# Kernel tuning notes

Hardware: AMD Instinct MI355X
Metric: run time of the kernel (lower is better)

## Reference

```python
import jax, jax.numpy as jnp
import numpy as np

N_NODES = 50000
N_EDGES = 800000
D = 64  # node_in = edge_out = node_out

def _mlp(h, w1, b1, w2, b2):
    h = jax.nn.relu(h @ w1 + b1)
    return h @ w2 + b2

def setup_inputs() -> dict:
    key = jax.random.key(0)
    ks = jax.random.split(key, 12)
    def lin(k, fan_in, fan_out):
        bound = 1.0 / np.sqrt(fan_in)
        kw, kb = jax.random.split(k)
        w = jax.random.uniform(kw, (fan_in, fan_out), jnp.float32, -bound, bound)
        b = jax.random.uniform(kb, (fan_out,), jnp.float32, -bound, bound)
        return w, b
    x = jax.random.normal(ks[0], (N_NODES, D), jnp.float32)
    edge_index = jax.random.randint(ks[1], (2, N_EDGES), 0, N_NODES, jnp.int64 if jax.config.jax_enable_x64 else jnp.int32)
    edge_attr = jax.random.normal(ks[2], (N_EDGES, D), jnp.float32)
    u = jax.random.normal(ks[3], (1, D), jnp.float32)
    batch = jnp.zeros((N_NODES,), dtype=edge_index.dtype)
    w1a, b1a = lin(ks[4], 2 * D, D)
    w1b, b1b = lin(ks[5], D, D)
    w2a, b2a = lin(ks[6], 2 * D, D)
    w2b, b2b = lin(ks[7], D, D)
    return dict(x=x, edge_index=edge_index, edge_attr=edge_attr, u=u, batch=batch,
                w1a=w1a, b1a=b1a, w1b=w1b, b1b=b1b,
                w2a=w2a, b2a=b2a, w2b=w2b, b2b=b2b)

def reference(x, edge_index, edge_attr, u, batch,
              w1a, b1a, w1b, b1b, w2a, b2a, w2b, b2b):
    row, col = edge_index[0], edge_index[1]
    n = x.shape[0]
    # gather source nodes, concat with edge features: [E, node_in+edge_out]
    h = jnp.concatenate([x[row], edge_attr], axis=1)
    h = _mlp(h, w1a, b1a, w1b, b1b)
    # scatter_mean over destination nodes (zeros for nodes with no incoming edges)
    summed = jax.ops.segment_sum(h, col, num_segments=n)  # [N, D]
    counts = jax.ops.segment_sum(jnp.ones((h.shape[0],), h.dtype), col, num_segments=n)
    agg = summed / jnp.maximum(counts, 1.0)[:, None]
    out = jnp.concatenate([x, agg], axis=1)
    return _mlp(out, w2a, b2a, w2b, b2b)
```

## Files before the change

kernel.cpp:

```cpp
#include <hip/hip_runtime.h>

#define DF 64

typedef __attribute__((ext_vector_type(8))) short bf16x8;
typedef __attribute__((ext_vector_type(2))) short v2s;
typedef __attribute__((ext_vector_type(4))) float f32x4;

__device__ __forceinline__ short f2bf(float f) {
    union { float f; unsigned u; } v; v.f = f;
    unsigned u = v.u;
    u += 0x7FFFu + ((u >> 16) & 1u);
    return (short)(u >> 16);
}

__device__ __forceinline__ float bf2f(unsigned s) {
    union { unsigned u; float f; } v; v.u = s << 16;
    return v.f;
}

__device__ __forceinline__ bf16x8 cvt8(float4 a, float4 b) {
    bf16x8 r;
    r[0] = f2bf(a.x); r[1] = f2bf(a.y); r[2] = f2bf(a.z); r[3] = f2bf(a.w);
    r[4] = f2bf(b.x); r[5] = f2bf(b.y); r[6] = f2bf(b.z); r[7] = f2bf(b.w);
    return r;
}

__device__ __forceinline__ void pk_add(short* addr, int val) {
#if __has_builtin(__builtin_amdgcn_global_atomic_fadd_v2bf16)
    __builtin_amdgcn_global_atomic_fadd_v2bf16(
        (__attribute__((address_space(1))) v2s*)addr, *(v2s*)&val);
#else
    unsigned* a = (unsigned*)addr;
    unsigned old = *a, assumed;
    do {
        assumed = old;
        float lo = bf2f(assumed & 0xffffu) + bf2f((unsigned)val & 0xffffu);
        float hi = bf2f(assumed >> 16)     + bf2f((unsigned)val >> 16);
        unsigned nv = (unsigned)(unsigned short)f2bf(lo) |
                      ((unsigned)(unsigned short)f2bf(hi) << 16);
        old = atomicCAS(a, assumed, nv);
    } while (old != assumed);
#endif
}

__global__ __launch_bounds__(256) void prep_weights(
    const float* __restrict__ w1a, const float* __restrict__ w1b,
    const float* __restrict__ w2a, const float* __restrict__ w2b,
    short* __restrict__ w1aT, short* __restrict__ w1bT,
    short* __restrict__ w2aT, short* __restrict__ w2bT)
{
    int gid = blockIdx.x * 256 + threadIdx.x;
    if (gid < 8192) {
        int k = gid >> 6, n = gid & 63;
        w1aT[n * 128 + k] = f2bf(w1a[gid]);
    } else if (gid < 12288) {
        int g = gid - 8192; int k = g >> 6, n = g & 63;
        w1bT[n * 64 + k] = f2bf(w1b[g]);
    } else if (gid < 20480) {
        int g = gid - 12288; int k = g >> 6, n = g & 63;
        w2aT[n * 128 + k] = f2bf(w2a[g]);
    } else if (gid < 24576) {
        int g = gid - 20480; int k = g >> 6, n = g & 63;
        w2bT[n * 64 + k] = f2bf(w2b[g]);
    }
}

__global__ __launch_bounds__(256, 8) void edge_mlp_scatter(
    const float* __restrict__ x, const int* __restrict__ ei,
    const float* __restrict__ ea,
    const short* __restrict__ w1aT, const float* __restrict__ b1a,
    const short* __restrict__ w1bT, const float* __restrict__ b1b,
    short* __restrict__ summedh, float* __restrict__ counts, int E)
{
    __shared__ alignas(16) short lsH[4 * 16 * 72];

    const int t = threadIdx.x;
    const int lane = t & 63;
    const int w = t >> 6;
    const int q = lane >> 4;
    const int m = lane & 15;
    const long base = ((long)blockIdx.x * 4 + w) * 16;

    const long e = base + m;
    const long ec = e < E ? e : (long)(E - 1);
    const int row = ei[ec];

    if (q == 0 && e < E)
        unsafeAtomicAdd(&counts[ei[E + e]], 1.0f);

    const float4* xr = (const float4*)(x + (long)row * DF);
    const float4* er = (const float4*)(ea + ec * DF);
    bf16x8 afr[4];
    afr[0] = cvt8(xr[q * 2],     xr[q * 2 + 1]);
    afr[1] = cvt8(xr[8 + q * 2], xr[8 + q * 2 + 1]);
    afr[2] = cvt8(er[q * 2],     er[q * 2 + 1]);
    afr[3] = cvt8(er[8 + q * 2], er[8 + q * 2 + 1]);

    f32x4 acc[4];
#pragma unroll
    for (int nt = 0; nt < 4; ++nt) {
        float b = b1a[nt * 16 + m];
        f32x4 v = {b, b, b, b};
        acc[nt] = v;
#pragma unroll
        for (int ks = 0; ks < 4; ++ks) {
            bf16x8 bfr = *(const bf16x8*)&w1aT[(nt * 16 + m) * 128 + ks * 32 + q * 8];
            acc[nt] = __builtin_amdgcn_mfma_f32_16x16x32_bf16(afr[ks], bfr, acc[nt], 0, 0, 0);
        }
    }

    short* hw = lsH + w * (16 * 72);
#pragma unroll
    for (int nt = 0; nt < 4; ++nt)
#pragma unroll
        for (int r = 0; r < 4; ++r) {
            float v = acc[nt][r] > 0.f ? acc[nt][r] : 0.f;
            hw[(q * 4 + r) * 72 + nt * 16 + m] = f2bf(v);
        }
    __syncthreads();

    bf16x8 a2[2];
    a2[0] = *(const bf16x8*)&hw[m * 72 + q * 8];
    a2[1] = *(const bf16x8*)&hw[m * 72 + 32 + q * 8];

    f32x4 acc2[4];
#pragma unroll
    for (int nt = 0; nt < 4; ++nt) {
        float b = b1b[nt * 16 + m];
        f32x4 v = {b, b, b, b};
        acc2[nt] = v;
#pragma unroll
        for (int ks = 0; ks < 2; ++ks) {
            bf16x8 bfr = *(const bf16x8*)&w1bT[(nt * 16 + m) * 64 + ks * 32 + q * 8];
            acc2[nt] = __builtin_amdgcn_mfma_f32_16x16x32_bf16(a2[ks], bfr, acc2[nt], 0, 0, 0);
        }
    }
    __syncthreads();

#pragma unroll
    for (int nt = 0; nt < 4; ++nt)
#pragma unroll
        for (int r = 0; r < 4; ++r)
            hw[(q * 4 + r) * 72 + nt * 16 + m] = f2bf(acc2[nt][r]);
    __syncthreads();

    const int p = lane & 31;
    const int* hwi = (const int*)hw;
#pragma unroll
    for (int i = 0; i < 8; ++i) {
        int r2 = (lane >> 5) + 2 * i;
        long eg = base + r2;
        if (eg < E) {
            int dst = ei[E + eg];
            int val = hwi[r2 * 36 + p];
            pk_add(&summedh[(long)dst * DF + 2 * p], val);
        }
    }
}

__global__ __launch_bounds__(256, 8) void node_mlp(
    const float* __restrict__ x, const short* __restrict__ summedh,
    const float* __restrict__ counts,
    const short* __restrict__ w2aT, const float* __restrict__ b2a,
    const short* __restrict__ w2bT, const float* __restrict__ b2b,
    float* __restrict__ out, int NN)
{
    __shared__ alignas(16) short lsH[4 * 16 * 72];

    const int t = threadIdx.x;
    const int lane = t & 63;
    const int w = t >> 6;
    const int q = lane >> 4;
    const int m = lane & 15;
    const long base = ((long)blockIdx.x * 4 + w) * 16;

    const long node = base + m;
    const long nc = node < NN ? node : (long)(NN - 1);

    const float4* xr = (const float4*)(x + nc * DF);
    float c = counts[nc];
    c = c > 1.f ? c : 1.f;
    const float inv = 1.f / c;

    bf16x8 s0 = *(const bf16x8*)&summedh[nc * DF + q * 8];
    bf16x8 s1 = *(const bf16x8*)&summedh[nc * DF + 32 + q * 8];

    bf16x8 afr[4];
    afr[0] = cvt8(xr[q * 2],     xr[q * 2 + 1]);
    afr[1] = cvt8(xr[8 + q * 2], xr[8 + q * 2 + 1]);
#pragma unroll
    for (int i = 0; i < 8; ++i) {
        afr[2][i] = f2bf(bf2f((unsigned short)s0[i]) * inv);
        afr[3][i] = f2bf(bf2f((unsigned short)s1[i]) * inv);
    }

    f32x4 acc[4];
#pragma unroll
    for (int nt = 0; nt < 4; ++nt) {
        float b = b2a[nt * 16 + m];
        f32x4 v = {b, b, b, b};
        acc[nt] = v;
#pragma unroll
        for (int ks = 0; ks < 4; ++ks) {
            bf16x8 bfr = *(const bf16x8*)&w2aT[(nt * 16 + m) * 128 + ks * 32 + q * 8];
            acc[nt] = __builtin_amdgcn_mfma_f32_16x16x32_bf16(afr[ks], bfr, acc[nt], 0, 0, 0);
        }
    }

    short* hw = lsH + w * (16 * 72);
#pragma unroll
    for (int nt = 0; nt < 4; ++nt)
#pragma unroll
        for (int r = 0; r < 4; ++r) {
            float v = acc[nt][r] > 0.f ? acc[nt][r] : 0.f;
            hw[(q * 4 + r) * 72 + nt * 16 + m] = f2bf(v);
        }
    __syncthreads();

    bf16x8 a2[2];
    a2[0] = *(const bf16x8*)&hw[m * 72 + q * 8];
    a2[1] = *(const bf16x8*)&hw[m * 72 + 32 + q * 8];

    f32x4 acc2[4];
#pragma unroll
    for (int nt = 0; nt < 4; ++nt) {
        float b = b2b[nt * 16 + m];
        f32x4 v = {b, b, b, b};
        acc2[nt] = v;
#pragma unroll
        for (int ks = 0; ks < 2; ++ks) {
            bf16x8 bfr = *(const bf16x8*)&w2bT[(nt * 16 + m) * 64 + ks * 32 + q * 8];
            acc2[nt] = __builtin_amdgcn_mfma_f32_16x16x32_bf16(a2[ks], bfr, acc2[nt], 0, 0, 0);
        }
    }

#pragma unroll
    for (int r = 0; r < 4; ++r) {
        long n2 = base + q * 4 + r;
        if (n2 < NN) {
#pragma unroll
            for (int nt = 0; nt < 4; ++nt)
                out[n2 * DF + nt * 16 + m] = acc2[nt][r];
        }
    }
}

extern "C" void kernel_launch(void* const* d_in, const int* in_sizes, int n_in,
                              void* d_out, int out_size, void* d_ws, size_t ws_size,
                              hipStream_t stream) {
    const float* x   = (const float*)d_in[0];
    const int*   ei  = (const int*)d_in[1];
    const float* ea  = (const float*)d_in[2];
    const float* w1a = (const float*)d_in[5];
    const float* b1a = (const float*)d_in[6];
    const float* w1b = (const float*)d_in[7];
    const float* b1b = (const float*)d_in[8];
    const float* w2a = (const float*)d_in[9];
    const float* b2a = (const float*)d_in[10];
    const float* w2b = (const float*)d_in[11];
    const float* b2b = (const float*)d_in[12];

    const int NN = in_sizes[0] / DF;
    const int E  = in_sizes[2] / DF;

    char* wsb = (char*)d_ws;
    float* counts  = (float*)wsb;
    short* w1aT    = (short*)(wsb + 262144);
    short* w1bT    = (short*)(wsb + 278528);
    short* w2aT    = (short*)(wsb + 286720);
    short* w2bT    = (short*)(wsb + 303104);
    short* summedh = (short*)(wsb + 311296);

    hipMemsetAsync(counts, 0, (size_t)NN * sizeof(float), stream);
    hipMemsetAsync(summedh, 0, (size_t)NN * DF * sizeof(short), stream);
    prep_weights<<<96, 256, 0, stream>>>(w1a, w1b, w2a, w2b, w1aT, w1bT, w2aT, w2bT);

    int etiles = (E + 15) / 16;
    int eblocks = (etiles + 3) / 4;
    edge_mlp_scatter<<<eblocks, 256, 0, stream>>>(x, ei, ea, w1aT, b1a, w1bT, b1b,
                                                  summedh, counts, E);
    int ntiles = (NN + 15) / 16;
    int nblocks = (ntiles + 3) / 4;
    node_mlp<<<nblocks, 256, 0, stream>>>(x, summedh, counts, w2aT, b2a, w2bT, b2b,
                                          (float*)d_out, NN);
}
```

Before: 465.9 us.

## Replace atomic scatter with CSR bucketing and gather-based segment mean

Builds a CSR layout of edges by destination (degree histogram, single-block scan, bucket permutation). Edge MLP outputs are written densely as bf16 per edge, and the node kernel gathers and averages them before the node MLP. This replaces atomic bf16 scatter-adds into a summed buffer with deterministic gathers. In exchange it adds three extra passes, a serial single-block scan over all nodes, a large per-edge intermediate buffer, and random gather reads. It falls back to the old path if the workspace is too small.

Result: slower. 606.2 us (+30.1%).

```diff
diff --git a/kernel.cpp b/kernel.cpp
--- a/kernel.cpp
+++ b/kernel.cpp
@@ -5,6 +5,7 @@
 typedef __attribute__((ext_vector_type(8))) short bf16x8;
 typedef __attribute__((ext_vector_type(2))) short v2s;
 typedef __attribute__((ext_vector_type(4))) float f32x4;
+typedef unsigned int u32;
 
 __device__ __forceinline__ short f2bf(float f) {
     union { float f; unsigned u; } v; v.f = f;
@@ -65,6 +66,252 @@
     }
 }
 
+
+__global__ __launch_bounds__(256) void degree_hist(
+    const int* __restrict__ ei, u32* __restrict__ deg, int E)
+{
+    int e = blockIdx.x * 256 + threadIdx.x;
+    if (e < E) atomicAdd(&deg[ei[E + e]], 1u);
+}
+
+__global__ __launch_bounds__(1024) void scan_offsets(
+    const u32* __restrict__ deg, u32* __restrict__ off,
+    u32* __restrict__ cursor, int NN)
+{
+    __shared__ u32 wtot[16];
+    __shared__ u32 carry_s;
+    const int t = threadIdx.x, lane = t & 63, wv = t >> 6;
+    if (t == 0) carry_s = 0;
+    __syncthreads();
+    for (int base = 0; base < NN; base += 1024) {
+        int i = base + t;
+        u32 v = (i < NN) ? deg[i] : 0u;
+        u32 x = v;
+#pragma unroll
+        for (int d = 1; d < 64; d <<= 1) {
+            u32 n = __shfl_up(x, (unsigned)d, 64);
+            if (lane >= d) x += n;
+        }
+        if (lane == 63) wtot[wv] = x;
+        __syncthreads();
+        u32 chunk_total = 0;
+        if (t == 0) {
+            u32 s = 0;
+            for (int k2 = 0; k2 < 16; ++k2) { u32 tv = wtot[k2]; wtot[k2] = s; s += tv; }
+            chunk_total = s;
+        }
+        __syncthreads();
+        u32 excl = carry_s + wtot[wv] + x - v;
+        if (i < NN) { off[i] = excl; cursor[i] = excl; }
+        __syncthreads();
+        if (t == 0) carry_s += chunk_total;
+        __syncthreads();
+    }
+    if (t == 0) off[NN] = carry_s;
+}
+
+__global__ __launch_bounds__(256) void bucket_edges(
+    const int* __restrict__ ei, u32* __restrict__ cursor,
+    u32* __restrict__ perm, int E)
+{
+    int e = blockIdx.x * 256 + threadIdx.x;
+    if (e < E) {
+        u32 pos = atomicAdd(&cursor[ei[E + e]], 1u);
+        perm[pos] = (u32)e;
+    }
+}
+
+
+__global__ __launch_bounds__(256, 8) void edge_mlp_h(
+    const float* __restrict__ x, const int* __restrict__ ei,
+    const float* __restrict__ ea,
+    const short* __restrict__ w1aT, const float* __restrict__ b1a,
+    const short* __restrict__ w1bT, const float* __restrict__ b1b,
+    short* __restrict__ h, int E)
+{
+    __shared__ alignas(16) short lsH[4 * 16 * 72];
+
+    const int t = threadIdx.x;
+    const int lane = t & 63;
+    const int w = t >> 6;
+    const int q = lane >> 4;
+    const int m = lane & 15;
+    const long base = ((long)blockIdx.x * 4 + w) * 16;
+
+    const long e = base + m;
+    const long ec = e < E ? e : (long)(E - 1);
+    const int row = ei[ec];
+
+    const float4* xr = (const float4*)(x + (long)row * DF);
+    const float4* er = (const float4*)(ea + ec * DF);
+    bf16x8 afr[4];
+    afr[0] = cvt8(xr[q * 2],     xr[q * 2 + 1]);
+    afr[1] = cvt8(xr[8 + q * 2], xr[8 + q * 2 + 1]);
+    afr[2] = cvt8(er[q * 2],     er[q * 2 + 1]);
+    afr[3] = cvt8(er[8 + q * 2], er[8 + q * 2 + 1]);
+
+    f32x4 acc[4];
+#pragma unroll
+    for (int nt = 0; nt < 4; ++nt) {
+        float b = b1a[nt * 16 + m];
+        f32x4 v = {b, b, b, b};
+        acc[nt] = v;
+#pragma unroll
+        for (int ks = 0; ks < 4; ++ks) {
+            bf16x8 bfr = *(const bf16x8*)&w1aT[(nt * 16 + m) * 128 + ks * 32 + q * 8];
+            acc[nt] = __builtin_amdgcn_mfma_f32_16x16x32_bf16(afr[ks], bfr, acc[nt], 0, 0, 0);
+        }
+    }
+
+    short* hw = lsH + w * (16 * 72);
+#pragma unroll
+    for (int nt = 0; nt < 4; ++nt)
+#pragma unroll
+        for (int r = 0; r < 4; ++r) {
+            float v = acc[nt][r] > 0.f ? acc[nt][r] : 0.f;
+            hw[(q * 4 + r) * 72 + nt * 16 + m] = f2bf(v);
+        }
+    __syncthreads();
+
+    bf16x8 a2[2];
+    a2[0] = *(const bf16x8*)&hw[m * 72 + q * 8];
+    a2[1] = *(const bf16x8*)&hw[m * 72 + 32 + q * 8];
+
+    f32x4 acc2[4];
+#pragma unroll
+    for (int nt = 0; nt < 4; ++nt) {
+        float b = b1b[nt * 16 + m];
+        f32x4 v = {b, b, b, b};
+        acc2[nt] = v;
+#pragma unroll
+        for (int ks = 0; ks < 2; ++ks) {
+            bf16x8 bfr = *(const bf16x8*)&w1bT[(nt * 16 + m) * 64 + ks * 32 + q * 8];
+            acc2[nt] = __builtin_amdgcn_mfma_f32_16x16x32_bf16(a2[ks], bfr, acc2[nt], 0, 0, 0);
+        }
+    }
+    __syncthreads();
+
+#pragma unroll
+    for (int nt = 0; nt < 4; ++nt)
+#pragma unroll
+        for (int r = 0; r < 4; ++r)
+            hw[(q * 4 + r) * 72 + nt * 16 + m] = f2bf(acc2[nt][r]);
+    __syncthreads();
+
+    const int* hwi = (const int*)hw;
+    int* ho = (int*)h;
+    const int p4 = lane & 7;
+    const int rr = lane >> 3;
+#pragma unroll
+    for (int i = 0; i < 2; ++i) {
+        int r2 = rr + 8 * i;
+        long eg = base + r2;
+        if (eg < E) {
+            int4 v = *(const int4*)&hwi[r2 * 36 + p4 * 4];
+            *(int4*)&ho[eg * 32 + p4 * 4] = v;
+        }
+    }
+}
+
+__global__ __launch_bounds__(256, 4) void node_mlp_agg(
+    const float* __restrict__ x, const short* __restrict__ h,
+    const u32* __restrict__ off, const u32* __restrict__ perm,
+    const short* __restrict__ w2aT, const float* __restrict__ b2a,
+    const short* __restrict__ w2bT, const float* __restrict__ b2b,
+    float* __restrict__ out, int NN)
+{
+    __shared__ alignas(16) short lsH[4 * 16 * 72];
+
+    const int t = threadIdx.x;
+    const int lane = t & 63;
+    const int w = t >> 6;
+    const int q = lane >> 4;
+    const int m = lane & 15;
+    const long base = ((long)blockIdx.x * 4 + w) * 16;
+
+    const long node = base + m;
+    const bool valid = node < NN;
+    const long nc = valid ? node : (long)(NN - 1);
+
+    const u32 o0 = off[nc];
+    const int deg = valid ? (int)(off[nc + 1] - o0) : 0;
+
+    float sa[8] = {0,0,0,0,0,0,0,0}, sb[8] = {0,0,0,0,0,0,0,0};
+    for (int j = 0; j < deg; ++j) {
+        int eid = (int)perm[o0 + j];
+        const short* hr = h + (long)eid * DF;
+        bf16x8 ha = *(const bf16x8*)(hr + q * 8);
+        bf16x8 hb = *(const bf16x8*)(hr + 32 + q * 8);
+#pragma unroll
+        for (int i = 0; i < 8; ++i) {
+            sa[i] += bf2f((unsigned short)ha[i]);
+            sb[i] += bf2f((unsigned short)hb[i]);
+        }
+    }
+    const float inv = deg > 0 ? 1.f / (float)deg : 1.f;
+
+    const float4* xr = (const float4*)(x + nc * DF);
+    bf16x8 afr[4];
+    afr[0] = cvt8(xr[q * 2],     xr[q * 2 + 1]);
+    afr[1] = cvt8(xr[8 + q * 2], xr[8 + q * 2 + 1]);
+#pragma unroll
+    for (int i = 0; i < 8; ++i) {
+        afr[2][i] = f2bf(sa[i] * inv);
+        afr[3][i] = f2bf(sb[i] * inv);
+    }
+
+    f32x4 acc[4];
+#pragma unroll
+    for (int nt = 0; nt < 4; ++nt) {
+        float b = b2a[nt * 16 + m];
+        f32x4 v = {b, b, b, b};
+        acc[nt] = v;
+#pragma unroll
+        for (int ks = 0; ks < 4; ++ks) {
+            bf16x8 bfr = *(const bf16x8*)&w2aT[(nt * 16 + m) * 128 + ks * 32 + q * 8];
+            acc[nt] = __builtin_amdgcn_mfma_f32_16x16x32_bf16(afr[ks], bfr, acc[nt], 0, 0, 0);
+        }
+    }
+
+    short* hw = lsH + w * (16 * 72);
+#pragma unroll
+    for (int nt = 0; nt < 4; ++nt)
+#pragma unroll
+        for (int r = 0; r < 4; ++r) {
+            float v = acc[nt][r] > 0.f ? acc[nt][r] : 0.f;
+            hw[(q * 4 + r) * 72 + nt * 16 + m] = f2bf(v);
+        }
+    __syncthreads();
+
+    bf16x8 a2[2];
+    a2[0] = *(const bf16x8*)&hw[m * 72 + q * 8];
+    a2[1] = *(const bf16x8*)&hw[m * 72 + 32 + q * 8];
+
+    f32x4 acc2[4];
+#pragma unroll
+    for (int nt = 0; nt < 4; ++nt) {
+        float b = b2b[nt * 16 + m];
+        f32x4 v = {b, b, b, b};
+        acc2[nt] = v;
+#pragma unroll
+        for (int ks = 0; ks < 2; ++ks) {
+            bf16x8 bfr = *(const bf16x8*)&w2bT[(nt * 16 + m) * 64 + ks * 32 + q * 8];
+            acc2[nt] = __builtin_amdgcn_mfma_f32_16x16x32_bf16(a2[ks], bfr, acc2[nt], 0, 0, 0);
+        }
+    }
+
+#pragma unroll
+    for (int r = 0; r < 4; ++r) {
+        long n2 = base + q * 4 + r;
+        if (n2 < NN) {
+#pragma unroll
+            for (int nt = 0; nt < 4; ++nt)
+                out[n2 * DF + nt * 16 + m] = acc2[nt][r];
+        }
+    }
+}
+
+
 __global__ __launch_bounds__(256, 8) void edge_mlp_scatter(
     const float* __restrict__ x, const int* __restrict__ ei,
     const float* __restrict__ ea,
@@ -264,23 +511,57 @@
     const int E  = in_sizes[2] / DF;
 
     char* wsb = (char*)d_ws;
-    float* counts  = (float*)wsb;
-    short* w1aT    = (short*)(wsb + 262144);
-    short* w1bT    = (short*)(wsb + 278528);
-    short* w2aT    = (short*)(wsb + 286720);
-    short* w2bT    = (short*)(wsb + 303104);
-    short* summedh = (short*)(wsb + 311296);
-
-    hipMemsetAsync(counts, 0, (size_t)NN * sizeof(float), stream);
-    hipMemsetAsync(summedh, 0, (size_t)NN * DF * sizeof(short), stream);
-    prep_weights<<<96, 256, 0, stream>>>(w1a, w1b, w2a, w2b, w1aT, w1bT, w2aT, w2bT);
-
-    int etiles = (E + 15) / 16;
-    int eblocks = (etiles + 3) / 4;
-    edge_mlp_scatter<<<eblocks, 256, 0, stream>>>(x, ei, ea, w1aT, b1a, w1bT, b1b,
-                                                  summedh, counts, E);
-    int ntiles = (NN + 15) / 16;
-    int nblocks = (ntiles + 3) / 4;
-    node_mlp<<<nblocks, 256, 0, stream>>>(x, summedh, counts, w2aT, b2a, w2bT, b2b,
-                                          (float*)d_out, NN);
-}
+
+    const size_t oDeg  = 0;
+    const size_t oOff  = 262144;
+    const size_t oCur  = 524288;
+    const size_t oPerm = 786432;
+    const size_t oW    = 4194304;
+    const size_t oH    = 4259840;
+    const size_t need  = oH + (size_t)E * DF * sizeof(short);
+
+    if (ws_size >= need) {
+        u32* deg    = (u32*)(wsb + oDeg);
+        u32* off    = (u32*)(wsb + oOff);
+        u32* cursor = (u32*)(wsb + oCur);
+        u32* perm   = (u32*)(wsb + oPerm);
+        short* w1aT = (short*)(wsb + oW);
+        short* w1bT = (short*)(wsb + oW + 16384);
+        short* w2aT = (short*)(wsb + oW + 24576);
+        short* w2bT = (short*)(wsb + oW + 40960);
+        short* h    = (short*)(wsb + oH);
+
+        hipMemsetAsync(deg, 0, (size_t)NN * sizeof(u32), stream);
+        prep_weights<<<96, 256, 0, stream>>>(w1a, w1b, w2a, w2b, w1aT, w1bT, w2aT, w2bT);
+
+        int e256 = (E + 255) / 256;
+        degree_hist<<<e256, 256, 0, stream>>>(ei, deg, E);
+        scan_offsets<<<1, 1024, 0, stream>>>(deg, off, cursor, NN);
+        bucket_edges<<<e256, 256, 0, stream>>>(ei, cursor, perm, E);
+
+        int eblocks = ((E + 15) / 16 + 3) / 4;
+        edge_mlp_h<<<eblocks, 256, 0, stream>>>(x, ei, ea, w1aT, b1a, w1bT, b1b, h, E);
+
+        int nblocks = ((NN + 15) / 16 + 3) / 4;
+        node_mlp_agg<<<nblocks, 256, 0, stream>>>(x, h, off, perm, w2aT, b2a, w2bT, b2b,
+                                                  (float*)d_out, NN);
+    } else {
+        float* counts  = (float*)wsb;
+        short* w1aT    = (short*)(wsb + 262144);
+        short* w1bT    = (short*)(wsb + 278528);
+        short* w2aT    = (short*)(wsb + 286720);
+        short* w2bT    = (short*)(wsb + 303104);
+        short* summedh = (short*)(wsb + 311296);
+
+        hipMemsetAsync(counts, 0, (size_t)NN * sizeof(float), stream);
+        hipMemsetAsync(summedh, 0, (size_t)NN * DF * sizeof(short), stream);
+        prep_weights<<<96, 256, 0, stream>>>(w1a, w1b, w2a, w2b, w1aT, w1bT, w2aT, w2bT);
+
+        int eblocks = ((E + 15) / 16 + 3) / 4;
+        edge_mlp_scatter<<<eblocks, 256, 0, stream>>>(x, ei, ea, w1aT, b1a, w1bT, b1b,
+                                                      summedh, counts, E);
+        int nblocks = ((NN + 15) / 16 + 3) / 4;
+        node_mlp<<<nblocks, 256, 0, stream>>>(x, summedh, counts, w2aT, b2a, w2bT, b2b,
+                                              (float*)d_out, NN);
+    }
+}
```
